# Optimization experiments

Measured on AMD Instinct MI355X. Metric: run time of the kernel, lower is better.

The kernel has to match this reference:

```python
import jax, jax.numpy as jnp
import numpy as np

S, I, H, O = 4096, 64, 1024, 1


def setup_inputs() -> dict:
    key = jax.random.key(0)
    ks = jax.random.split(key, 8)
    k = 1.0 / np.sqrt(H)  # torch LSTM/Linear init scale
    u = lambda kk, shp: jax.random.uniform(kk, shp, jnp.float32, -k, k)
    return {
        "input_seq": jax.random.normal(ks[0], (S, I), jnp.float32),
        "W_ih": u(ks[1], (4 * H, I)),
        "W_hh": u(ks[2], (4 * H, H)),
        "b_ih": u(ks[3], (4 * H,)),
        "b_hh": u(ks[4], (4 * H,)),
        "W_lin": u(ks[5], (O, H)),
        "b_lin": u(ks[6], (O,)),
    }


def reference(input_seq, W_ih, W_hh, b_ih, b_hh, W_lin, b_lin):
    # Precompute input contributions to all gates in one GEMM: [S, 4H]
    x_gates = input_seq @ W_ih.T + (b_ih + b_hh)

    def step(carry, xg):
        h, c = carry
        g = xg + h @ W_hh.T  # [4H], gate order i, f, g, o (torch convention)
        i, f, gg, o = jnp.split(g, 4)
        i = jax.nn.sigmoid(i)
        f = jax.nn.sigmoid(f)
        gg = jnp.tanh(gg)
        o = jax.nn.sigmoid(o)
        c = f * c + i * gg
        h = o * jnp.tanh(c)
        return (h, c), None

    h0 = jnp.zeros((H,), x_gates.dtype)
    c0 = jnp.zeros((H,), x_gates.dtype)
    (h_last, _), _ = jax.lax.scan(step, (h0, c0), x_gates)
    # original applies linear to every step then takes [-1]; equivalent to
    # projecting only the last hidden state
    return h_last @ W_lin.T + b_lin  # [O]
```

## Files before the change

kernel.cpp:

```cpp
#include <hip/hip_runtime.h>


#define SEQ_LEN 4096
#define HID 1024
#define NBLK 128
#define TPB 512
#define HPB 8

__device__ __forceinline__ float fast_sigmoid(float x) {
    return __builtin_amdgcn_rcpf(1.0f + __builtin_amdgcn_exp2f(-1.4426950408889634f * x));
}
__device__ __forceinline__ float fast_tanh(float x) {
    return fmaf(-2.0f, __builtin_amdgcn_rcpf(1.0f + __builtin_amdgcn_exp2f(2.8853900817779268f * x)), 1.0f);
}

__global__ void lstm_init_kernel(unsigned long long* ws) {
    int t = threadIdx.x;
    #pragma unroll
    for (int k = 0; k < 8; ++k) ws[t + 256 * k] = 0ull;
}

__global__ __launch_bounds__(TPB, 1) void lstm_persistent_kernel(
    const float* __restrict__ input,
    const float* __restrict__ W_ih,
    const float* __restrict__ W_hh,
    const float* __restrict__ b_ih,
    const float* __restrict__ b_hh,
    const float* __restrict__ W_lin,
    const float* __restrict__ b_lin,
    float* __restrict__ out,
    unsigned long long* __restrict__ ws)
{
    const int t   = threadIdx.x;
    const int b   = blockIdx.x;
    const int w   = t >> 6;
    const int l   = t & 63;
    const int grp = l >> 4;
    const int sl  = l & 15;
    const int j   = HPB * b + w;
    const int row = grp * HID + j;

    unsigned long long* slot0 = ws;
    unsigned long long* slot1 = ws + HID;

    __shared__ float4 wlds4[17 * TPB];
    __shared__ float  hs[2][HID];
    __shared__ unsigned long long pub[HPB];
    __shared__ float  red[HPB];

    {
        const float4* Whh4 = (const float4*)(W_hh + (size_t)row * HID);
        #pragma unroll
        for (int c = 0; c < 16; ++c)
            wlds4[c * TPB + t] = Whh4[sl + 16 * c];
        wlds4[16 * TPB + t] = ((const float4*)(W_ih + (size_t)row * 64))[sl];
    }
    float bias[4];
    #pragma unroll
    for (int q = 0; q < 4; ++q) bias[q] = b_ih[q * HID + j] + b_hh[q * HID + j];
    if (t < HPB) pub[t] = 0ull;

    const float4* xin4 = (const float4*)input;
    float c_state = 0.0f;
    __syncthreads();

    for (int s = 0; s < SEQ_LEN; ++s) {
        float4 x4 = xin4[s * 16 + sl];

        unsigned long long* rs = (s & 1) ? slot1 : slot0;
        const unsigned tag = (unsigned)s;
        unsigned long long v0, v1;
        bool r0 = false, r1 = false;
        do {
            if (!r0) { v0 = __hip_atomic_load(&rs[t      ], __ATOMIC_RELAXED, __HIP_MEMORY_SCOPE_AGENT);
                       r0 = ((unsigned)(v0 >> 32) == tag); }
            if (!r1) { v1 = __hip_atomic_load(&rs[t + 512], __ATOMIC_RELAXED, __HIP_MEMORY_SCOPE_AGENT);
                       r1 = ((unsigned)(v1 >> 32) == tag); }
        } while (!(r0 && r1));

        float* hsb = hs[s & 1];
        hsb[t      ] = __uint_as_float((unsigned)(v0 & 0xffffffffull));
        hsb[t + 512] = __uint_as_float((unsigned)(v1 & 0xffffffffull));

        __syncthreads();

        const float4* hs4 = (const float4*)hsb;
        float a0 = 0.f, a1 = 0.f, a2 = 0.f, a3 = 0.f;
        #pragma unroll
        for (int c = 0; c < 16; c += 4) {
            float4 wv0 = wlds4[(c    ) * TPB + t], h40 = hs4[16 * (c    ) + sl];
            float4 wv1 = wlds4[(c + 1) * TPB + t], h41 = hs4[16 * (c + 1) + sl];
            float4 wv2 = wlds4[(c + 2) * TPB + t], h42 = hs4[16 * (c + 2) + sl];
            float4 wv3 = wlds4[(c + 3) * TPB + t], h43 = hs4[16 * (c + 3) + sl];
            a0 = fmaf(wv0.x, h40.x, a0); a0 = fmaf(wv0.y, h40.y, a0);
            a0 = fmaf(wv0.z, h40.z, a0); a0 = fmaf(wv0.w, h40.w, a0);
            a1 = fmaf(wv1.x, h41.x, a1); a1 = fmaf(wv1.y, h41.y, a1);
            a1 = fmaf(wv1.z, h41.z, a1); a1 = fmaf(wv1.w, h41.w, a1);
            a2 = fmaf(wv2.x, h42.x, a2); a2 = fmaf(wv2.y, h42.y, a2);
            a2 = fmaf(wv2.z, h42.z, a2); a2 = fmaf(wv2.w, h42.w, a2);
            a3 = fmaf(wv3.x, h43.x, a3); a3 = fmaf(wv3.y, h43.y, a3);
            a3 = fmaf(wv3.z, h43.z, a3); a3 = fmaf(wv3.w, h43.w, a3);
        }
        {
            float4 wv = wlds4[16 * TPB + t];
            a0 = fmaf(wv.x, x4.x, a0); a1 = fmaf(wv.y, x4.y, a1);
            a2 = fmaf(wv.z, x4.z, a2); a3 = fmaf(wv.w, x4.w, a3);
        }
        float acc = (a0 + a1) + (a2 + a3);

        acc += __shfl_xor(acc, 1);
        acc += __shfl_xor(acc, 2);
        acc += __shfl_xor(acc, 4);
        acc += __shfl_xor(acc, 8);

        float gi = __shfl(acc, 0)  + bias[0];
        float gf = __shfl(acc, 16) + bias[1];
        float gg = __shfl(acc, 32) + bias[2];
        float go = __shfl(acc, 48) + bias[3];

        float ig = fast_sigmoid(gi);
        float fg = fast_sigmoid(gf);
        float cg = fast_tanh(gg);
        float og = fast_sigmoid(go);
        c_state  = fmaf(fg, c_state, ig * cg);
        float hn = og * fast_tanh(c_state);

        const unsigned ntag = (unsigned)(s + 1);
        if (l == 0) {
            unsigned long long pv = ((unsigned long long)ntag << 32) |
                                    (unsigned long long)__float_as_uint(hn);
            __hip_atomic_store(&pub[w], pv, __ATOMIC_RELAXED, __HIP_MEMORY_SCOPE_WORKGROUP);
        }
        if (w == 0 && l < HPB) {
            unsigned long long pv;
            do {
                pv = __hip_atomic_load(&pub[l], __ATOMIC_RELAXED, __HIP_MEMORY_SCOPE_WORKGROUP);
            } while ((unsigned)(pv >> 32) != ntag);
            unsigned long long* wsl = (s & 1) ? slot0 : slot1;
            __hip_atomic_store(&wsl[HPB * b + l], pv, __ATOMIC_RELAXED, __HIP_MEMORY_SCOPE_AGENT);
        }
    }

    if (b == 0) {
        const unsigned tag = (unsigned)SEQ_LEN;
        unsigned long long v0, v1;
        bool r0 = false, r1 = false;
        do {
            if (!r0) { v0 = __hip_atomic_load(&slot0[t      ], __ATOMIC_RELAXED, __HIP_MEMORY_SCOPE_AGENT);
                       r0 = ((unsigned)(v0 >> 32) == tag); }
            if (!r1) { v1 = __hip_atomic_load(&slot0[t + 512], __ATOMIC_RELAXED, __HIP_MEMORY_SCOPE_AGENT);
                       r1 = ((unsigned)(v1 >> 32) == tag); }
        } while (!(r0 && r1));
        float p = __uint_as_float((unsigned)(v0 & 0xffffffffull)) * W_lin[t] +
                  __uint_as_float((unsigned)(v1 & 0xffffffffull)) * W_lin[t + 512];
        #pragma unroll
        for (int m = 32; m >= 1; m >>= 1) p += __shfl_xor(p, m);
        if (l == 0) red[w] = p;
        __syncthreads();
        if (t == 0) {
            float r = 0.f;
            #pragma unroll
            for (int k = 0; k < HPB; ++k) r += red[k];
            out[0] = r + b_lin[0];
        }
    }
}

extern "C" void kernel_launch(void* const* d_in, const int* in_sizes, int n_in,
                              void* d_out, int out_size, void* d_ws, size_t ws_size,
                              hipStream_t stream) {
    const float* input = (const float*)d_in[0];
    const float* W_ih  = (const float*)d_in[1];
    const float* W_hh  = (const float*)d_in[2];
    const float* b_ih  = (const float*)d_in[3];
    const float* b_hh  = (const float*)d_in[4];
    const float* W_lin = (const float*)d_in[5];
    const float* b_lin = (const float*)d_in[6];
    float* out = (float*)d_out;
    unsigned long long* ws = (unsigned long long*)d_ws;

    hipLaunchKernelGGL(lstm_init_kernel, dim3(1), dim3(256), 0, stream, ws);

    void* args[] = { (void*)&input, (void*)&W_ih, (void*)&W_hh, (void*)&b_ih,
                     (void*)&b_hh, (void*)&W_lin, (void*)&b_lin, (void*)&out, (void*)&ws };
    (void)hipLaunchCooperativeKernel((void*)lstm_persistent_kernel, dim3(NBLK), dim3(TPB),
                                     args, 0, stream);
}
```

Baseline: 8.416 ms.

## Add dedicated loader warp per block and drop block-wide barrier per step

Adds a 65th... rather, a ninth wavefront per block that alone polls the global h slots, copies them into the double-buffered shared h array and signals readiness through a shared flag. The eight compute wavefronts spin on that flag instead of a __syncthreads, and each publishes its own h value straight to global memory rather than funnelling through wave 0. The goal is to take the cross-block poll and the block barrier off the compute waves' critical path. In exchange, the compute waves spin on shared memory, there is an extra wavefront, and the double buffer now relies only on the acquire/release flags with no explicit barrier guarding reuse.

```diff
diff --git a/kernel.cpp b/kernel.cpp
--- a/kernel.cpp
+++ b/kernel.cpp
@@ -4,7 +4,7 @@
 #define SEQ_LEN 4096
 #define HID 1024
 #define NBLK 128
-#define TPB 512
+#define TPB 576
 #define HPB 8
 
 __device__ __forceinline__ float fast_sigmoid(float x) {
@@ -31,137 +31,142 @@
     float* __restrict__ out,
     unsigned long long* __restrict__ ws)
 {
-    const int t   = threadIdx.x;
-    const int b   = blockIdx.x;
-    const int w   = t >> 6;
-    const int l   = t & 63;
-    const int grp = l >> 4;
-    const int sl  = l & 15;
-    const int j   = HPB * b + w;
-    const int row = grp * HID + j;
+    const int t = threadIdx.x;
+    const int b = blockIdx.x;
+    const int w = t >> 6;
+    const int l = t & 63;
 
     unsigned long long* slot0 = ws;
     unsigned long long* slot1 = ws + HID;
 
-    __shared__ float4 wlds4[17 * TPB];
+    __shared__ float4 wlds4[17 * 512];
     __shared__ float  hs[2][HID];
-    __shared__ unsigned long long pub[HPB];
-    __shared__ float  red[HPB];
+    __shared__ unsigned hready[2];
 
-    {
+    const int tc  = t - 64;
+    const int grp = l >> 4;
+    const int sl  = l & 15;
+    const int j   = HPB * b + (w - 1);
+    const int row = grp * HID + j;
+
+    float bias[4];
+    if (w > 0) {
         const float4* Whh4 = (const float4*)(W_hh + (size_t)row * HID);
         #pragma unroll
         for (int c = 0; c < 16; ++c)
-            wlds4[c * TPB + t] = Whh4[sl + 16 * c];
-        wlds4[16 * TPB + t] = ((const float4*)(W_ih + (size_t)row * 64))[sl];
+            wlds4[c * 512 + tc] = Whh4[sl + 16 * c];
+        wlds4[16 * 512 + tc] = ((const float4*)(W_ih + (size_t)row * 64))[sl];
+        #pragma unroll
+        for (int q = 0; q < 4; ++q) bias[q] = b_ih[q * HID + j] + b_hh[q * HID + j];
     }
-    float bias[4];
-    #pragma unroll
-    for (int q = 0; q < 4; ++q) bias[q] = b_ih[q * HID + j] + b_hh[q * HID + j];
-    if (t < HPB) pub[t] = 0ull;
-
-    const float4* xin4 = (const float4*)input;
-    float c_state = 0.0f;
+    if (t < 2) hready[t] = 0u;
     __syncthreads();
 
-    for (int s = 0; s < SEQ_LEN; ++s) {
-        float4 x4 = xin4[s * 16 + sl];
+    if (w == 0) {
+        for (int s = 0; s < SEQ_LEN; ++s) {
+            unsigned long long* rs = (s & 1) ? slot1 : slot0;
+            const unsigned tag = (unsigned)s;
+            float* hsb = hs[s & 1];
+            unsigned long long v[16];
+            bool ok;
+            do {
+                #pragma unroll
+                for (int k = 0; k < 16; ++k)
+                    v[k] = __hip_atomic_load(&rs[l + 64 * k], __ATOMIC_RELAXED,
+                                             __HIP_MEMORY_SCOPE_AGENT);
+                ok = true;
+                #pragma unroll
+                for (int k = 0; k < 16; ++k)
+                    ok = ok && ((unsigned)(v[k] >> 32) == tag);
+            } while (!__all(ok));
+            #pragma unroll
+            for (int k = 0; k < 16; ++k)
+                hsb[l + 64 * k] = __uint_as_float((unsigned)(v[k] & 0xffffffffull));
+            if (l == 0)
+                __hip_atomic_store(&hready[s & 1], (unsigned)(s + 1),
+                                   __ATOMIC_RELEASE, __HIP_MEMORY_SCOPE_WORKGROUP);
+        }
+        if (b == 0) {
+            const unsigned tag = (unsigned)SEQ_LEN;
+            unsigned long long v[16];
+            bool ok;
+            do {
+                #pragma unroll
+                for (int k = 0; k < 16; ++k)
+                    v[k] = __hip_atomic_load(&slot0[l + 64 * k], __ATOMIC_RELAXED,
+                                             __HIP_MEMORY_SCOPE_AGENT);
+                ok = true;
+                #pragma unroll
+                for (int k = 0; k < 16; ++k)
+                    ok = ok && ((unsigned)(v[k] >> 32) == tag);
+            } while (!__all(ok));
+            float p = 0.0f;
+            #pragma unroll
+            for (int k = 0; k < 16; ++k)
+                p = fmaf(__uint_as_float((unsigned)(v[k] & 0xffffffffull)),
+                         W_lin[l + 64 * k], p);
+            #pragma unroll
+            for (int m = 32; m >= 1; m >>= 1) p += __shfl_xor(p, m);
+            if (l == 0) out[0] = p + b_lin[0];
+        }
+    } else {
+        const float4* xin4 = (const float4*)input;
+        float c_state = 0.0f;
+        for (int s = 0; s < SEQ_LEN; ++s) {
+            float4 x4 = xin4[s * 16 + sl];
 
-        unsigned long long* rs = (s & 1) ? slot1 : slot0;
-        const unsigned tag = (unsigned)s;
-        unsigned long long v0, v1;
-        bool r0 = false, r1 = false;
-        do {
-            if (!r0) { v0 = __hip_atomic_load(&rs[t      ], __ATOMIC_RELAXED, __HIP_MEMORY_SCOPE_AGENT);
-                       r0 = ((unsigned)(v0 >> 32) == tag); }
-            if (!r1) { v1 = __hip_atomic_load(&rs[t + 512], __ATOMIC_RELAXED, __HIP_MEMORY_SCOPE_AGENT);
-                       r1 = ((unsigned)(v1 >> 32) == tag); }
-        } while (!(r0 && r1));
+            const unsigned need = (unsigned)(s + 1);
+            while (__hip_atomic_load(&hready[s & 1], __ATOMIC_ACQUIRE,
+                                     __HIP_MEMORY_SCOPE_WORKGROUP) < need) {}
 
-        float* hsb = hs[s & 1];
-        hsb[t      ] = __uint_as_float((unsigned)(v0 & 0xffffffffull));
-        hsb[t + 512] = __uint_as_float((unsigned)(v1 & 0xffffffffull));
+            const float4* hs4 = (const float4*)hs[s & 1];
+            float a0 = 0.f, a1 = 0.f, a2 = 0.f, a3 = 0.f;
+            #pragma unroll
+            for (int c = 0; c < 16; c += 4) {
+                float4 wv0 = wlds4[(c    ) * 512 + tc], h40 = hs4[16 * (c    ) + sl];
+                float4 wv1 = wlds4[(c + 1) * 512 + tc], h41 = hs4[16 * (c + 1) + sl];
+                float4 wv2 = wlds4[(c + 2) * 512 + tc], h42 = hs4[16 * (c + 2) + sl];
+                float4 wv3 = wlds4[(c + 3) * 512 + tc], h43 = hs4[16 * (c + 3) + sl];
+                a0 = fmaf(wv0.x, h40.x, a0); a0 = fmaf(wv0.y, h40.y, a0);
+                a0 = fmaf(wv0.z, h40.z, a0); a0 = fmaf(wv0.w, h40.w, a0);
+                a1 = fmaf(wv1.x, h41.x, a1); a1 = fmaf(wv1.y, h41.y, a1);
+                a1 = fmaf(wv1.z, h41.z, a1); a1 = fmaf(wv1.w, h41.w, a1);
+                a2 = fmaf(wv2.x, h42.x, a2); a2 = fmaf(wv2.y, h42.y, a2);
+                a2 = fmaf(wv2.z, h42.z, a2); a2 = fmaf(wv2.w, h42.w, a2);
+                a3 = fmaf(wv3.x, h43.x, a3); a3 = fmaf(wv3.y, h43.y, a3);
+                a3 = fmaf(wv3.z, h43.z, a3); a3 = fmaf(wv3.w, h43.w, a3);
+            }
+            {
+                float4 wv = wlds4[16 * 512 + tc];
+                a0 = fmaf(wv.x, x4.x, a0); a1 = fmaf(wv.y, x4.y, a1);
+                a2 = fmaf(wv.z, x4.z, a2); a3 = fmaf(wv.w, x4.w, a3);
+            }
+            float acc = (a0 + a1) + (a2 + a3);
 
-        __syncthreads();
+            acc += __shfl_xor(acc, 1);
+            acc += __shfl_xor(acc, 2);
+            acc += __shfl_xor(acc, 4);
+            acc += __shfl_xor(acc, 8);
 
-        const float4* hs4 = (const float4*)hsb;
-        float a0 = 0.f, a1 = 0.f, a2 = 0.f, a3 = 0.f;
-        #pragma unroll
-        for (int c = 0; c < 16; c += 4) {
-            float4 wv0 = wlds4[(c    ) * TPB + t], h40 = hs4[16 * (c    ) + sl];
-            float4 wv1 = wlds4[(c + 1) * TPB + t], h41 = hs4[16 * (c + 1) + sl];
-            float4 wv2 = wlds4[(c + 2) * TPB + t], h42 = hs4[16 * (c + 2) + sl];
-            float4 wv3 = wlds4[(c + 3) * TPB + t], h43 = hs4[16 * (c + 3) + sl];
-            a0 = fmaf(wv0.x, h40.x, a0); a0 = fmaf(wv0.y, h40.y, a0);
-            a0 = fmaf(wv0.z, h40.z, a0); a0 = fmaf(wv0.w, h40.w, a0);
-            a1 = fmaf(wv1.x, h41.x, a1); a1 = fmaf(wv1.y, h41.y, a1);
-            a1 = fmaf(wv1.z, h41.z, a1); a1 = fmaf(wv1.w, h41.w, a1);
-            a2 = fmaf(wv2.x, h42.x, a2); a2 = fmaf(wv2.y, h42.y, a2);
-            a2 = fmaf(wv2.z, h42.z, a2); a2 = fmaf(wv2.w, h42.w, a2);
-            a3 = fmaf(wv3.x, h43.x, a3); a3 = fmaf(wv3.y, h43.y, a3);
-            a3 = fmaf(wv3.z, h43.z, a3); a3 = fmaf(wv3.w, h43.w, a3);
-        }
-        {
-            float4 wv = wlds4[16 * TPB + t];
-            a0 = fmaf(wv.x, x4.x, a0); a1 = fmaf(wv.y, x4.y, a1);
-            a2 = fmaf(wv.z, x4.z, a2); a3 = fmaf(wv.w, x4.w, a3);
-        }
-        float acc = (a0 + a1) + (a2 + a3);
+            float gi = __shfl(acc, 0)  + bias[0];
+            float gf = __shfl(acc, 16) + bias[1];
+            float gg = __shfl(acc, 32) + bias[2];
+            float go = __shfl(acc, 48) + bias[3];
 
-        acc += __shfl_xor(acc, 1);
-        acc += __shfl_xor(acc, 2);
-        acc += __shfl_xor(acc, 4);
-        acc += __shfl_xor(acc, 8);
+            float ig = fast_sigmoid(gi);
+            float fg = fast_sigmoid(gf);
+            float cg = fast_tanh(gg);
+            float og = fast_sigmoid(go);
+            c_state  = fmaf(fg, c_state, ig * cg);
+            float hn = og * fast_tanh(c_state);
 
-        float gi = __shfl(acc, 0)  + bias[0];
-        float gf = __shfl(acc, 16) + bias[1];
-        float gg = __shfl(acc, 32) + bias[2];
-        float go = __shfl(acc, 48) + bias[3];
-
-        float ig = fast_sigmoid(gi);
-        float fg = fast_sigmoid(gf);
-        float cg = fast_tanh(gg);
-        float og = fast_sigmoid(go);
-        c_state  = fmaf(fg, c_state, ig * cg);
-        float hn = og * fast_tanh(c_state);
-
-        const unsigned ntag = (unsigned)(s + 1);
-        if (l == 0) {
-            unsigned long long pv = ((unsigned long long)ntag << 32) |
-                                    (unsigned long long)__float_as_uint(hn);
-            __hip_atomic_store(&pub[w], pv, __ATOMIC_RELAXED, __HIP_MEMORY_SCOPE_WORKGROUP);
-        }
-        if (w == 0 && l < HPB) {
-            unsigned long long pv;
-            do {
-                pv = __hip_atomic_load(&pub[l], __ATOMIC_RELAXED, __HIP_MEMORY_SCOPE_WORKGROUP);
-            } while ((unsigned)(pv >> 32) != ntag);
-            unsigned long long* wsl = (s & 1) ? slot0 : slot1;
-            __hip_atomic_store(&wsl[HPB * b + l], pv, __ATOMIC_RELAXED, __HIP_MEMORY_SCOPE_AGENT);
-        }
-    }
-
-    if (b == 0) {
-        const unsigned tag = (unsigned)SEQ_LEN;
-        unsigned long long v0, v1;
-        bool r0 = false, r1 = false;
-        do {
-            if (!r0) { v0 = __hip_atomic_load(&slot0[t      ], __ATOMIC_RELAXED, __HIP_MEMORY_SCOPE_AGENT);
-                       r0 = ((unsigned)(v0 >> 32) == tag); }
-            if (!r1) { v1 = __hip_atomic_load(&slot0[t + 512], __ATOMIC_RELAXED, __HIP_MEMORY_SCOPE_AGENT);
-                       r1 = ((unsigned)(v1 >> 32) == tag); }
-        } while (!(r0 && r1));
-        float p = __uint_as_float((unsigned)(v0 & 0xffffffffull)) * W_lin[t] +
-                  __uint_as_float((unsigned)(v1 & 0xffffffffull)) * W_lin[t + 512];
-        #pragma unroll
-        for (int m = 32; m >= 1; m >>= 1) p += __shfl_xor(p, m);
-        if (l == 0) red[w] = p;
-        __syncthreads();
-        if (t == 0) {
-            float r = 0.f;
-            #pragma unroll
-            for (int k = 0; k < HPB; ++k) r += red[k];
-            out[0] = r + b_lin[0];
+            if (l == 0) {
+                unsigned long long pv = ((unsigned long long)need << 32) |
+                                        (unsigned long long)__float_as_uint(hn);
+                unsigned long long* wsl = (s & 1) ? slot0 : slot1;
+                __hip_atomic_store(&wsl[j], pv, __ATOMIC_RELAXED,
+                                   __HIP_MEMORY_SCOPE_AGENT);
+            }
         }
     }
 }
```

After: 13.40 ms. 59.2% more time.

## Add dedicated publisher wavefront per block to forward hidden state globally

Applied to the files above, without the earlier changes.

Adds a ninth wavefront per block that only waits on the per-wave LDS publish slots and forwards the tagged hidden values to the global exchange buffer, running at raised priority. The eight compute waves no longer have wave 0 doing publishing work on the critical path, so they can start polling for the next step sooner. The publisher wave joins each step's barrier, which couples it to the compute waves' sync and adds one more wave's scheduling overhead per step.

```diff
diff --git a/kernel.cpp b/kernel.cpp
--- a/kernel.cpp
+++ b/kernel.cpp
@@ -4,7 +4,7 @@
 #define SEQ_LEN 4096
 #define HID 1024
 #define NBLK 128
-#define TPB 512
+#define TPB 576
 #define HPB 8
 
 __device__ __forceinline__ float fast_sigmoid(float x) {
@@ -31,128 +31,142 @@
     float* __restrict__ out,
     unsigned long long* __restrict__ ws)
 {
-    const int t   = threadIdx.x;
-    const int b   = blockIdx.x;
-    const int w   = t >> 6;
-    const int l   = t & 63;
+    const int t = threadIdx.x;
+    const int b = blockIdx.x;
+    const int w = t >> 6;
+    const int l = t & 63;
+
+    unsigned long long* slot0 = ws;
+    unsigned long long* slot1 = ws + HID;
+
+    __shared__ float4 wlds4[17 * 512];
+    __shared__ float  hs[2][HID];
+    __shared__ unsigned long long pub[HPB];
+    __shared__ float  red[16];
+
+    const int tc  = t - 64;
     const int grp = l >> 4;
     const int sl  = l & 15;
-    const int j   = HPB * b + w;
+    const int j   = HPB * b + (w - 1);
     const int row = grp * HID + j;
 
-    unsigned long long* slot0 = ws;
-    unsigned long long* slot1 = ws + HID;
-
-    __shared__ float4 wlds4[17 * TPB];
-    __shared__ float  hs[2][HID];
-    __shared__ unsigned long long pub[HPB];
-    __shared__ float  red[HPB];
-
-    {
+    float bias[4];
+    if (w > 0) {
         const float4* Whh4 = (const float4*)(W_hh + (size_t)row * HID);
         #pragma unroll
         for (int c = 0; c < 16; ++c)
-            wlds4[c * TPB + t] = Whh4[sl + 16 * c];
-        wlds4[16 * TPB + t] = ((const float4*)(W_ih + (size_t)row * 64))[sl];
+            wlds4[c * 512 + tc] = Whh4[sl + 16 * c];
+        wlds4[16 * 512 + tc] = ((const float4*)(W_ih + (size_t)row * 64))[sl];
+        #pragma unroll
+        for (int q = 0; q < 4; ++q) bias[q] = b_ih[q * HID + j] + b_hh[q * HID + j];
     }
-    float bias[4];
-    #pragma unroll
-    for (int q = 0; q < 4; ++q) bias[q] = b_ih[q * HID + j] + b_hh[q * HID + j];
     if (t < HPB) pub[t] = 0ull;
-
-    const float4* xin4 = (const float4*)input;
-    float c_state = 0.0f;
     __syncthreads();
 
-    for (int s = 0; s < SEQ_LEN; ++s) {
-        float4 x4 = xin4[s * 16 + sl];
-
-        unsigned long long* rs = (s & 1) ? slot1 : slot0;
-        const unsigned tag = (unsigned)s;
-        unsigned long long v0, v1;
-        bool r0 = false, r1 = false;
-        do {
-            if (!r0) { v0 = __hip_atomic_load(&rs[t      ], __ATOMIC_RELAXED, __HIP_MEMORY_SCOPE_AGENT);
-                       r0 = ((unsigned)(v0 >> 32) == tag); }
-            if (!r1) { v1 = __hip_atomic_load(&rs[t + 512], __ATOMIC_RELAXED, __HIP_MEMORY_SCOPE_AGENT);
-                       r1 = ((unsigned)(v1 >> 32) == tag); }
-        } while (!(r0 && r1));
-
-        float* hsb = hs[s & 1];
-        hsb[t      ] = __uint_as_float((unsigned)(v0 & 0xffffffffull));
-        hsb[t + 512] = __uint_as_float((unsigned)(v1 & 0xffffffffull));
-
-        __syncthreads();
-
-        const float4* hs4 = (const float4*)hsb;
-        float a0 = 0.f, a1 = 0.f, a2 = 0.f, a3 = 0.f;
-        #pragma unroll
-        for (int c = 0; c < 16; c += 4) {
-            float4 wv0 = wlds4[(c    ) * TPB + t], h40 = hs4[16 * (c    ) + sl];
-            float4 wv1 = wlds4[(c + 1) * TPB + t], h41 = hs4[16 * (c + 1) + sl];
-            float4 wv2 = wlds4[(c + 2) * TPB + t], h42 = hs4[16 * (c + 2) + sl];
-            float4 wv3 = wlds4[(c + 3) * TPB + t], h43 = hs4[16 * (c + 3) + sl];
-            a0 = fmaf(wv0.x, h40.x, a0); a0 = fmaf(wv0.y, h40.y, a0);
-            a0 = fmaf(wv0.z, h40.z, a0); a0 = fmaf(wv0.w, h40.w, a0);
-            a1 = fmaf(wv1.x, h41.x, a1); a1 = fmaf(wv1.y, h41.y, a1);
-            a1 = fmaf(wv1.z, h41.z, a1); a1 = fmaf(wv1.w, h41.w, a1);
-            a2 = fmaf(wv2.x, h42.x, a2); a2 = fmaf(wv2.y, h42.y, a2);
-            a2 = fmaf(wv2.z, h42.z, a2); a2 = fmaf(wv2.w, h42.w, a2);
-            a3 = fmaf(wv3.x, h43.x, a3); a3 = fmaf(wv3.y, h43.y, a3);
-            a3 = fmaf(wv3.z, h43.z, a3); a3 = fmaf(wv3.w, h43.w, a3);
-        }
-        {
-            float4 wv = wlds4[16 * TPB + t];
-            a0 = fmaf(wv.x, x4.x, a0); a1 = fmaf(wv.y, x4.y, a1);
-            a2 = fmaf(wv.z, x4.z, a2); a3 = fmaf(wv.w, x4.w, a3);
-        }
-        float acc = (a0 + a1) + (a2 + a3);
-
-        acc += __shfl_xor(acc, 1);
-        acc += __shfl_xor(acc, 2);
-        acc += __shfl_xor(acc, 4);
-        acc += __shfl_xor(acc, 8);
-
-        float gi = __shfl(acc, 0)  + bias[0];
-        float gf = __shfl(acc, 16) + bias[1];
-        float gg = __shfl(acc, 32) + bias[2];
-        float go = __shfl(acc, 48) + bias[3];
-
-        float ig = fast_sigmoid(gi);
-        float fg = fast_sigmoid(gf);
-        float cg = fast_tanh(gg);
-        float og = fast_sigmoid(go);
-        c_state  = fmaf(fg, c_state, ig * cg);
-        float hn = og * fast_tanh(c_state);
-
-        const unsigned ntag = (unsigned)(s + 1);
-        if (l == 0) {
-            unsigned long long pv = ((unsigned long long)ntag << 32) |
-                                    (unsigned long long)__float_as_uint(hn);
-            __hip_atomic_store(&pub[w], pv, __ATOMIC_RELAXED, __HIP_MEMORY_SCOPE_WORKGROUP);
-        }
-        if (w == 0 && l < HPB) {
-            unsigned long long pv;
+    if (w == 0) {
+        asm volatile("s_setprio 1");
+        for (int s = 0; s < SEQ_LEN; ++s) {
+            __syncthreads();
+            const unsigned ntag = (unsigned)(s + 1);
+            unsigned long long pv = 0;
+            if (l < HPB) {
+                do {
+                    pv = __hip_atomic_load(&pub[l], __ATOMIC_RELAXED,
+                                           __HIP_MEMORY_SCOPE_WORKGROUP);
+                } while ((unsigned)(pv >> 32) != ntag);
+                unsigned long long* wsl = (s & 1) ? slot0 : slot1;
+                __hip_atomic_store(&wsl[HPB * b + l], pv, __ATOMIC_RELAXED,
+                                   __HIP_MEMORY_SCOPE_AGENT);
+            }
+        }
+    } else {
+        const float4* xin4 = (const float4*)input;
+        float c_state = 0.0f;
+        for (int s = 0; s < SEQ_LEN; ++s) {
+            float4 x4 = xin4[s * 16 + sl];
+
+            unsigned long long* rs = (s & 1) ? slot1 : slot0;
+            const unsigned tag = (unsigned)s;
+            unsigned long long v0, v1;
+            bool r0 = false, r1 = false;
             do {
-                pv = __hip_atomic_load(&pub[l], __ATOMIC_RELAXED, __HIP_MEMORY_SCOPE_WORKGROUP);
-            } while ((unsigned)(pv >> 32) != ntag);
-            unsigned long long* wsl = (s & 1) ? slot0 : slot1;
-            __hip_atomic_store(&wsl[HPB * b + l], pv, __ATOMIC_RELAXED, __HIP_MEMORY_SCOPE_AGENT);
+                if (!r0) { v0 = __hip_atomic_load(&rs[tc      ], __ATOMIC_RELAXED, __HIP_MEMORY_SCOPE_AGENT);
+                           r0 = ((unsigned)(v0 >> 32) == tag); }
+                if (!r1) { v1 = __hip_atomic_load(&rs[tc + 512], __ATOMIC_RELAXED, __HIP_MEMORY_SCOPE_AGENT);
+                           r1 = ((unsigned)(v1 >> 32) == tag); }
+            } while (!(r0 && r1));
+
+            float* hsb = hs[s & 1];
+            hsb[tc      ] = __uint_as_float((unsigned)(v0 & 0xffffffffull));
+            hsb[tc + 512] = __uint_as_float((unsigned)(v1 & 0xffffffffull));
+
+            __syncthreads();
+
+            const float4* hs4 = (const float4*)hsb;
+            float a0 = 0.f, a1 = 0.f, a2 = 0.f, a3 = 0.f;
+            #pragma unroll
+            for (int c = 0; c < 16; c += 4) {
+                float4 wv0 = wlds4[(c    ) * 512 + tc], h40 = hs4[16 * (c    ) + sl];
+                float4 wv1 = wlds4[(c + 1) * 512 + tc], h41 = hs4[16 * (c + 1) + sl];
+                float4 wv2 = wlds4[(c + 2) * 512 + tc], h42 = hs4[16 * (c + 2) + sl];
+                float4 wv3 = wlds4[(c + 3) * 512 + tc], h43 = hs4[16 * (c + 3) + sl];
+                a0 = fmaf(wv0.x, h40.x, a0); a0 = fmaf(wv0.y, h40.y, a0);
+                a0 = fmaf(wv0.z, h40.z, a0); a0 = fmaf(wv0.w, h40.w, a0);
+                a1 = fmaf(wv1.x, h41.x, a1); a1 = fmaf(wv1.y, h41.y, a1);
+                a1 = fmaf(wv1.z, h41.z, a1); a1 = fmaf(wv1.w, h41.w, a1);
+                a2 = fmaf(wv2.x, h42.x, a2); a2 = fmaf(wv2.y, h42.y, a2);
+                a2 = fmaf(wv2.z, h42.z, a2); a2 = fmaf(wv2.w, h42.w, a2);
+                a3 = fmaf(wv3.x, h43.x, a3); a3 = fmaf(wv3.y, h43.y, a3);
+                a3 = fmaf(wv3.z, h43.z, a3); a3 = fmaf(wv3.w, h43.w, a3);
+            }
+            {
+                float4 wv = wlds4[16 * 512 + tc];
+                a0 = fmaf(wv.x, x4.x, a0); a1 = fmaf(wv.y, x4.y, a1);
+                a2 = fmaf(wv.z, x4.z, a2); a3 = fmaf(wv.w, x4.w, a3);
+            }
+            float acc = (a0 + a1) + (a2 + a3);
+
+            acc += __shfl_xor(acc, 1);
+            acc += __shfl_xor(acc, 2);
+            acc += __shfl_xor(acc, 4);
+            acc += __shfl_xor(acc, 8);
+
+            float gi = __shfl(acc, 0)  + bias[0];
+            float gf = __shfl(acc, 16) + bias[1];
+            float gg = __shfl(acc, 32) + bias[2];
+            float go = __shfl(acc, 48) + bias[3];
+
+            float ig = fast_sigmoid(gi);
+            float fg = fast_sigmoid(gf);
+            float cg = fast_tanh(gg);
+            float og = fast_sigmoid(go);
+            c_state  = fmaf(fg, c_state, ig * cg);
+            float hn = og * fast_tanh(c_state);
+
+            if (l == 0) {
+                unsigned long long pv = ((unsigned long long)(unsigned)(s + 1) << 32) |
+                                        (unsigned long long)__float_as_uint(hn);
+                __hip_atomic_store(&pub[w - 1], pv, __ATOMIC_RELAXED,
+                                   __HIP_MEMORY_SCOPE_WORKGROUP);
+            }
         }
     }
 
     if (b == 0) {
-        const unsigned tag = (unsigned)SEQ_LEN;
-        unsigned long long v0, v1;
-        bool r0 = false, r1 = false;
-        do {
-            if (!r0) { v0 = __hip_atomic_load(&slot0[t      ], __ATOMIC_RELAXED, __HIP_MEMORY_SCOPE_AGENT);
-                       r0 = ((unsigned)(v0 >> 32) == tag); }
-            if (!r1) { v1 = __hip_atomic_load(&slot0[t + 512], __ATOMIC_RELAXED, __HIP_MEMORY_SCOPE_AGENT);
-                       r1 = ((unsigned)(v1 >> 32) == tag); }
-        } while (!(r0 && r1));
-        float p = __uint_as_float((unsigned)(v0 & 0xffffffffull)) * W_lin[t] +
-                  __uint_as_float((unsigned)(v1 & 0xffffffffull)) * W_lin[t + 512];
+        float p = 0.0f;
+        if (w > 0) {
+            const unsigned tag = (unsigned)SEQ_LEN;
+            unsigned long long v0, v1;
+            bool r0 = false, r1 = false;
+            do {
+                if (!r0) { v0 = __hip_atomic_load(&slot0[tc      ], __ATOMIC_RELAXED, __HIP_MEMORY_SCOPE_AGENT);
+                           r0 = ((unsigned)(v0 >> 32) == tag); }
+                if (!r1) { v1 = __hip_atomic_load(&slot0[tc + 512], __ATOMIC_RELAXED, __HIP_MEMORY_SCOPE_AGENT);
+                           r1 = ((unsigned)(v1 >> 32) == tag); }
+            } while (!(r0 && r1));
+            p = __uint_as_float((unsigned)(v0 & 0xffffffffull)) * W_lin[tc] +
+                __uint_as_float((unsigned)(v1 & 0xffffffffull)) * W_lin[tc + 512];
+        }
         #pragma unroll
         for (int m = 32; m >= 1; m >>= 1) p += __shfl_xor(p, m);
         if (l == 0) red[w] = p;
@@ -160,7 +174,7 @@
         if (t == 0) {
             float r = 0.f;
             #pragma unroll
-            for (int k = 0; k < HPB; ++k) r += red[k];
+            for (int k = 1; k <= HPB; ++k) r += red[k];
             out[0] = r + b_lin[0];
         }
     }
```

Result: slower. 8.806 ms (+4.6%).
